# Performance work log

Hardware: AMD Instinct MI355X
Metric: run time of the kernel (lower is better)

The kernel has to match this reference:

```python
import jax, jax.numpy as jnp
import numpy as np

V, E, H, L = 50257, 256, 1024, 2   # vocab, embed_dim, hidden_dim, num_layers
B, T, K = 64, 80, 5                # batch, max_len, top_k
TEMP = 0.75
TWO_PI_OVER_24 = np.float32(2.0 * np.pi / 24.0)


def setup_inputs() -> dict:
    key = jax.random.key(0)
    ks = jax.random.split(key, 12)
    n = lambda i, shape, s: (jax.random.normal(ks[i], shape, jnp.float32) * s)
    hours = jax.random.uniform(ks[0], (B,), jnp.float32) * 24.0
    return {
        "hours": hours,
        "tp_w1": n(1, (2, H), 0.5),
        "tp_b1": jnp.zeros((H,), jnp.float32),
        "tp_w2": n(2, (H, 2 * L * H), 0.02),
        "tp_b2": jnp.zeros((2 * L * H,), jnp.float32),
        "embed": n(3, (V, E), 0.1).at[0].set(0.0),  # padding_idx=0 row zeroed
        "w_ih0": n(4, (E, 4 * H), 0.05),
        "w_hh0": n(5, (H, 4 * H), 0.05),
        "b0": jnp.zeros((4 * H,), jnp.float32),     # b_ih + b_hh combined
        "w_ih1": n(6, (H, 4 * H), 0.05),
        "w_hh1": n(7, (H, 4 * H), 0.05),
        "b1": jnp.zeros((4 * H,), jnp.float32),
        "fc_w": n(8, (H, V), 0.02),
        "fc_b": jnp.zeros((V,), jnp.float32),
        "sos_id": 1,
    }


def _lstm_cell(x, h, c, w_ih, w_hh, b):
    # torch gate order: i, f, g, o
    g = x @ w_ih + h @ w_hh + b
    i, f, gg, o = jnp.split(g, 4, axis=-1)
    c2 = jax.nn.sigmoid(f) * c + jax.nn.sigmoid(i) * jnp.tanh(gg)
    h2 = jax.nn.sigmoid(o) * jnp.tanh(c2)
    return h2, c2


def reference(hours, tp_w1, tp_b1, tp_w2, tp_b2, embed,
              w_ih0, w_hh0, b0, w_ih1, w_hh1, b1, fc_w, fc_b, sos_id):
    # _encode_time: sin/cos of hour angle -> MLP -> (h0, c0) per layer
    a = hours * TWO_PI_OVER_24
    feat = jnp.stack([jnp.sin(a), jnp.cos(a)], axis=-1)          # [B,2]
    tp = jnp.tanh(feat @ tp_w1 + tp_b1) @ tp_w2 + tp_b2          # [B,2*L*H]
    tp = tp.reshape(B, L, 2, H)
    h = jnp.transpose(tp[:, :, 0, :], (1, 0, 2))                 # [L,B,H]
    c = jnp.transpose(tp[:, :, 1, :], (1, 0, 2))                 # [L,B,H]

    keys = jax.random.split(jax.random.key(42), T)

    def step(carry, k):
        h, c, tok = carry
        x = embed[tok]                                           # [B,E]
        h0n, c0n = _lstm_cell(x, h[0], c[0], w_ih0, w_hh0, b0)
        h1n, c1n = _lstm_cell(h0n, h[1], c[1], w_ih1, w_hh1, b1)
        logits = (h1n @ fc_w + fc_b) / TEMP                      # [B,V]
        topv, topi = jax.lax.top_k(logits, K)                    # [B,K]
        probs = jax.nn.softmax(topv, axis=-1)
        sel = jax.random.categorical(k, topv, axis=-1)           # [B], == multinomial(probs)
        nxt = jnp.take_along_axis(topi, sel[:, None], axis=1)[:, 0]
        return (jnp.stack([h0n, h1n]), jnp.stack([c0n, c1n]), nxt), (nxt, probs)

    tok0 = jnp.full((B,), sos_id, jnp.int32)
    _, (toks, probs) = jax.lax.scan(step, (h, c, tok0), keys)
    # toks: [T,B] -> [B,T]; probs: [T,B,K] -> [B,T,K]
    return jnp.transpose(toks, (1, 0)), jnp.transpose(probs, (1, 0, 2))
```

## Files before the change

kernel.cpp:

```cpp
#include <hip/hip_runtime.h>
#include <math.h>
#include <stdint.h>
#include <limits.h>

#define VSZ 50257
#define ESZ 256
#define HSZ 1024
#define BSZ 64
#define TSZ 80
#define GC  4096
#define NFCB 786
#define NCAND (NFCB*5)
#define NSLOT 13
#define NREF 16

typedef unsigned int u32;
typedef unsigned short u16;
typedef double f64x4 __attribute__((ext_vector_type(4)));
typedef float f32x4v __attribute__((ext_vector_type(4)));
typedef __bf16 bf16x8 __attribute__((ext_vector_type(8)));
union BFrag { u16 u[8]; bf16x8 v; };

__device__ __forceinline__ u16 f2bf(float f) {
  u32 x = __float_as_uint(f);
  return (u16)((x + 0x7FFFu + ((x >> 16) & 1u)) >> 16);
}
__device__ __forceinline__ float bf2f(u16 h) { return __uint_as_float(((u32)h) << 16); }

__device__ __forceinline__ void tf2x32(u32 k0, u32 k1, u32& x0, u32& x1) {
  u32 ks2 = k0 ^ k1 ^ 0x1BD11BDAu;
  x0 += k0; x1 += k1;
#define RND(r) { x0 += x1; x1 = (x1 << r) | (x1 >> (32 - r)); x1 ^= x0; }
  RND(13) RND(15) RND(26) RND(6)
  x0 += k1; x1 += ks2 + 1u;
  RND(17) RND(29) RND(16) RND(24)
  x0 += ks2; x1 += k0 + 2u;
  RND(13) RND(15) RND(26) RND(6)
  x0 += k0; x1 += k1 + 3u;
  RND(17) RND(29) RND(16) RND(24)
  x0 += k1; x1 += ks2 + 4u;
  RND(13) RND(15) RND(26) RND(6)
  x0 += ks2; x1 += k0 + 5u;
#undef RND
}

__device__ __forceinline__ double dsig(double x) { return 0.5 + 0.5 * tanh(0.5 * x); }

__device__ __forceinline__ void ins5(double v, int i, double* tv, int* ti) {
  bool beat4 = (v > tv[4]) || (v == tv[4] && i < ti[4]);
  if (!beat4) return;
  tv[4] = v; ti[4] = i;
#pragma unroll
  for (int p = 4; p > 0; --p) {
    bool sw = (tv[p] > tv[p-1]) || (tv[p] == tv[p-1] && ti[p] < ti[p-1]);
    double a0 = sw ? tv[p] : tv[p-1]; double a1 = sw ? tv[p-1] : tv[p];
    tv[p-1] = a0; tv[p] = a1;
    int b0 = sw ? ti[p] : ti[p-1]; int b1 = sw ? ti[p-1] : ti[p];
    ti[p-1] = b0; ti[p] = b1;
  }
}

__device__ __forceinline__ double dref(int m, int n) {
  int s = 0;
#pragma unroll
  for (int k = 0; k < 4; ++k) s += (4*m + k + 1) * (16*k + n + 1);
  return (double)s;
}

__global__ __launch_bounds__(64) void k_probe(int* __restrict__ fbp) {
  int l = threadIdx.x;
  int lane16 = l & 15, sub = l >> 4;
  {
    double av = (double)(4 * lane16 + sub + 1);
    double bv = (double)(16 * sub + lane16 + 1);
    f64x4 acc = {0., 0., 0., 0.};
    acc = __builtin_amdgcn_mfma_f64_16x16x4f64(av, bv, acc, 0, 0, 0);
    bool o0 = true, o1 = true, o2 = true, o3 = true;
#pragma unroll
    for (int j = 0; j < 4; ++j) {
      double d = acc[j];
      o0 = o0 && (d == dref(4 * sub + j, lane16));
      o1 = o1 && (d == dref(lane16, 4 * sub + j));
      o2 = o2 && (d == dref(sub + 4 * j, lane16));
      o3 = o3 && (d == dref(lane16, sub + 4 * j));
    }
    int a0 = __all(o0), a1 = __all(o1), a2 = __all(o2), a3 = __all(o3);
    if (l == 0) { fbp[0] = a0 ? 0 : a1 ? 1 : a2 ? 2 : 3; fbp[1] = 0; }
  }
  {
    BFrag fa, fbv;
#pragma unroll
    for (int i = 0; i < 8; ++i) {
      int k = sub * 8 + i;
      fa.u[i]  = f2bf((float)((lane16 * 5 + k * 3) % 63 + 1));
      fbv.u[i] = f2bf((float)((k * 7 + lane16 * 11) % 61 + 1));
    }
    f32x4v c = {0.f, 0.f, 0.f, 0.f};
    c = __builtin_amdgcn_mfma_f32_16x16x32_bf16(fa.v, fbv.v, c, 0, 0, 0);
    bool okb = true;
#pragma unroll
    for (int j = 0; j < 4; ++j) {
      int mm = sub * 4 + j, nn = lane16;
      int ref = 0;
      for (int k = 0; k < 32; ++k) ref += ((mm*5 + k*3) % 63 + 1) * ((k*7 + nn*11) % 61 + 1);
      okb = okb && (c[j] == (float)ref);
    }
    int allb = __all(okb);
    if (l == 0) fbp[2] = allb;
  }
}

__global__ __launch_bounds__(256) void k_wconv(const float* __restrict__ W, u16* __restrict__ whT) {
  __shared__ u16 tile[64][65];
  int vb = blockIdx.x * 64, kb = blockIdx.y * 64;
  int tid = threadIdx.x;
#pragma unroll
  for (int i = 0; i < 16; ++i) {
    int r = i * 4 + (tid >> 6), c = tid & 63;
    int v = vb + c;
    tile[c][r] = (v < VSZ) ? f2bf(W[(size_t)(kb + r) * VSZ + v]) : (u16)0;
  }
  __syncthreads();
#pragma unroll
  for (int i = 0; i < 16; ++i) {
    int r = i * 4 + (tid >> 6), c = tid & 63;
    int v = vb + r;
    if (v < VSZ) whT[(size_t)v * 1024 + kb + c] = tile[r][c];
  }
}

__global__ __launch_bounds__(256) void k_rng(double* __restrict__ gum) {
  int idx = blockIdx.x * 256 + threadIdx.x;
  if (idx >= TSZ * 320) return;
  int t = idx / 320, m = idx % 320;
  u32 a0 = 0u, a1 = (u32)t;
  tf2x32(0u, 42u, a0, a1);
  u32 x0 = 0u, x1 = (u32)m;
  tf2x32(a0, a1, x0, x1);
  u32 bits = x0 ^ x1;
  const float TINY = 1.17549435082228750797e-38f;
  float f = __uint_as_float((bits >> 9) | 0x3f800000u) - 1.0f;
  float u = f + TINY;
  u = fmaxf(TINY, u);
  gum[idx] = -log(-log((double)u));
}

__global__ __launch_bounds__(256) void k_time1(const float* __restrict__ hours, const float* __restrict__ w1,
                                               const float* __restrict__ bb1, double* __restrict__ tp1T) {
  int idx = blockIdx.x * 256 + threadIdx.x;
  int b = idx & 63, hcol = idx >> 6;
  const float TPO = (float)(2.0 * 3.14159265358979323846 / 24.0);
  float af = hours[b] * TPO;
  double a = (double)af;
  double sv = sin(a), cv = cos(a);
  double vv = tanh(sv * (double)w1[hcol] + cv * (double)w1[HSZ + hcol] + (double)bb1[hcol]);
  tp1T[(size_t)hcol * 64 + b] = vv;
}

__global__ __launch_bounds__(256) void k_gemm_simple(const double* __restrict__ XTa, const float* __restrict__ Wa,
                                                     int Ka, int Sa, double* __restrict__ part) {
  int j = blockIdx.x * 256 + threadIdx.x;
  if (j >= GC) return;
  int s = blockIdx.y;
  int kc = Ka / Sa, k0 = s * kc;
  double acc[BSZ];
#pragma unroll
  for (int b = 0; b < BSZ; ++b) acc[b] = 0.0;
  const float* wp = Wa + (size_t)k0 * GC + j;
  const double* xp = XTa + (size_t)k0 * 64;
  for (int k = 0; k < kc; ++k) {
    double wv = (double)wp[0]; wp += GC;
#pragma unroll
    for (int b = 0; b < BSZ; ++b) acc[b] = fma(wv, xp[b], acc[b]);
    xp += 64;
  }
  double* o = part + ((size_t)s * 64) * GC + j;
#pragma unroll
  for (int b = 0; b < BSZ; ++b) o[(size_t)b * GC] = acc[b];
}

__global__ __launch_bounds__(256) void k_t2r(const double* __restrict__ part, const float* __restrict__ b2,
                                             double* __restrict__ h0T, double* __restrict__ c0,
                                             double* __restrict__ h1T, double* __restrict__ c1) {
  int b = blockIdx.y;
  int j = blockIdx.x * 256 + threadIdx.x;
  double acc = (double)b2[j];
  for (int s = 0; s < 8; ++s) acc += part[((size_t)s * 64 + b) * GC + j];
  int l = j >> 11, half = (j >> 10) & 1, hcol = j & 1023;
  if (half == 0) (l ? h1T : h0T)[(size_t)hcol * 64 + b] = acc;
  else           (l ? c1 : c0)[(size_t)b * HSZ + hcol] = acc;
}

__global__ __launch_bounds__(256, 4) void k_lstm_mfma(const double* __restrict__ x0, const float* __restrict__ W0,
                                                      const double* __restrict__ x1, const float* __restrict__ W1,
                                                      const double* __restrict__ x2, const float* __restrict__ W2,
                                                      int s1, int s2, double* __restrict__ part,
                                                      const int* __restrict__ fbp) {
  int conv = fbp[0] & 3;
  __shared__ double xs[64 * 64];
  int tid = threadIdx.x;
  int l = tid & 63, wv = tid >> 6;
  int sub = l >> 4, lane16 = l & 15;
  int colbase = blockIdx.x * 64;
  int s = blockIdx.y;
  const double* XT; const float* W; int k0;
  if (s < s1)      { XT = x0; W = W0; k0 = s * 256; }
  else if (s < s2) { XT = x1; W = W1; k0 = (s - s1) * 256; }
  else             { XT = x2; W = W2; k0 = (s - s2) * 256; }
  int colA = colbase + wv * 16 + lane16;
  f64x4 a0 = {0.,0.,0.,0.}, a1 = {0.,0.,0.,0.}, a2 = {0.,0.,0.,0.}, a3 = {0.,0.,0.,0.};
  const float* wp = W + (size_t)(k0 + sub) * GC + colA;
  float ab[8];
#pragma unroll
  for (int u = 0; u < 8; ++u) { ab[u] = wp[0]; wp += (size_t)4 * GC; }
  for (int ch = 0; ch < 4; ++ch) {
    __syncthreads();
    const double2* src = (const double2*)(XT + (size_t)(k0 + ch * 64) * 64);
    double2* dst = (double2*)xs;
    for (int i = tid; i < 2048; i += 256) dst[i] = src[i];
    __syncthreads();
#pragma unroll
    for (int g = 0; g < 2; ++g) {
#pragma unroll
      for (int u = 0; u < 8; ++u) {
        int ks = g * 8 + u;
        int step = ch * 16 + ks;
        float nv = 0.f;
        if (step + 8 < 64) nv = wp[0];
        wp += (size_t)4 * GC;
        double av = (double)ab[u];
        const double* bp = xs + (ks * 4 + sub) * 64 + lane16;
        double b0 = bp[0], b1 = bp[16], b2 = bp[32], b3 = bp[48];
        a0 = __builtin_amdgcn_mfma_f64_16x16x4f64(av, b0, a0, 0, 0, 0);
        a1 = __builtin_amdgcn_mfma_f64_16x16x4f64(av, b1, a1, 0, 0, 0);
        a2 = __builtin_amdgcn_mfma_f64_16x16x4f64(av, b2, a2, 0, 0, 0);
        a3 = __builtin_amdgcn_mfma_f64_16x16x4f64(av, b3, a3, 0, 0, 0);
        ab[u] = nv;
      }
    }
  }
#pragma unroll
  for (int j = 0; j < 4; ++j) {
    int m = (conv == 0) ? sub * 4 + j : (conv == 2) ? sub + 4 * j : lane16;
    int n = (conv == 0) ? lane16 : (conv == 2) ? lane16 : ((conv == 1) ? sub * 4 + j : sub + 4 * j);
    size_t base = ((size_t)s * 64 + n) * GC + colbase + wv * 16 + m;
    part[base]                   = a0[j];
    part[base + (size_t)16 * GC] = a1[j];
    part[base + (size_t)32 * GC] = a2[j];
    part[base + (size_t)48 * GC] = a3[j];
  }
}

__global__ __launch_bounds__(256) void k_cell(const double* __restrict__ part, int sBeg, int S,
                                              const float* __restrict__ bias,
                                              double* __restrict__ c, double* __restrict__ hT,
                                              int emit, u16* __restrict__ xh) {
  int b = blockIdx.y;
  int hcol = blockIdx.x * 256 + threadIdx.x;
  double gi = (double)bias[hcol];
  double gf = (double)bias[1024 + hcol];
  double gg = (double)bias[2048 + hcol];
  double go = (double)bias[3072 + hcol];
#pragma unroll 4
  for (int s = sBeg; s < sBeg + S; ++s) {
    const double* p = part + ((size_t)s * 64 + b) * GC;
    gi += p[hcol]; gf += p[1024 + hcol]; gg += p[2048 + hcol]; go += p[3072 + hcol];
  }
  size_t ci = (size_t)b * HSZ + hcol;
  double cn = dsig(gf) * c[ci] + dsig(gi) * tanh(gg);
  double hn = dsig(go) * tanh(cn);
  c[ci] = cn;
  hT[(size_t)hcol * 64 + b] = hn;
  if (emit)
    xh[(size_t)(hcol >> 7) * 8192 + (size_t)b * 128 + (hcol & 127)] = f2bf((float)hn);
}

__global__ __launch_bounds__(256, 4) void k_fcbf(const u16* __restrict__ xhg, const u16* __restrict__ whT,
                                                 const float* __restrict__ fcb,
                                                 double* __restrict__ candV, int* __restrict__ candI,
                                                 const int* __restrict__ fbp) {
  if (fbp[2] == 0) return;
  __shared__ double xs[64 * 64];
  u16* lx = (u16*)xs;
  int tid = threadIdx.x;
  int l = tid & 63, wv = tid >> 6;
  int sub = l >> 4, lane16 = l & 15;
  int vbase = blockIdx.x * 64;
  int colA = min(vbase + wv * 16 + lane16, VSZ - 1);
  const u16* wrow = whT + (size_t)colA * 1024;
  f32x4v acc0 = {0,0,0,0}, acc1 = {0,0,0,0}, acc2 = {0,0,0,0}, acc3 = {0,0,0,0};
  for (int ch = 0; ch < 8; ++ch) {
    bf16x8 wh0 = *(const bf16x8*)(wrow + ch * 128 + 0 * 32 + sub * 8);
    bf16x8 wh1 = *(const bf16x8*)(wrow + ch * 128 + 1 * 32 + sub * 8);
    bf16x8 wh2 = *(const bf16x8*)(wrow + ch * 128 + 2 * 32 + sub * 8);
    bf16x8 wh3 = *(const bf16x8*)(wrow + ch * 128 + 3 * 32 + sub * 8);
    __syncthreads();
    {
      const uint4* sg = (const uint4*)(xhg + (size_t)ch * 8192);
      uint4* dl = (uint4*)lx;
#pragma unroll
      for (int i = 0; i < 4; ++i) {
        int u = tid + i * 256;
        int bswz = u >> 4, g = u & 15;
        dl[(bswz << 4) | (g ^ (bswz & 7))] = sg[u];
      }
    }
    __syncthreads();
#pragma unroll
    for (int kt = 0; kt < 4; ++kt) {
      bf16x8 whv = (kt == 0) ? wh0 : (kt == 1) ? wh1 : (kt == 2) ? wh2 : wh3;
#define BT_STEP(BT, ACC) {                                                              \
        int bb = BT * 16 + lane16;                                                      \
        const bf16x8* bp2 = (const bf16x8*)lx + ((bb << 4) | ((kt * 4 + sub) ^ (bb & 7))); \
        ACC = __builtin_amdgcn_mfma_f32_16x16x32_bf16(whv, *bp2, ACC, 0, 0, 0); }
      BT_STEP(0, acc0)
      BT_STEP(1, acc1)
      BT_STEP(2, acc2)
      BT_STEP(3, acc3)
#undef BT_STEP
    }
  }
  __syncthreads();
#pragma unroll
  for (int j = 0; j < 4; ++j) {
    int vl = wv * 16 + sub * 4 + j;
    int v = vbase + vl;
    bool okv = (v < VSZ);
    double bi = okv ? (double)fcb[min(v, VSZ - 1)] : 0.0;
    int b0i = lane16, b1i = 16 + lane16, b2i = 32 + lane16, b3i = 48 + lane16;
    xs[b0i * 64 + ((vl + b0i) & 63)] = okv ? ((double)acc0[j] + bi) / 0.75 : -INFINITY;
    xs[b1i * 64 + ((vl + b1i) & 63)] = okv ? ((double)acc1[j] + bi) / 0.75 : -INFINITY;
    xs[b2i * 64 + ((vl + b2i) & 63)] = okv ? ((double)acc2[j] + bi) / 0.75 : -INFINITY;
    xs[b3i * 64 + ((vl + b3i) & 63)] = okv ? ((double)acc3[j] + bi) / 0.75 : -INFINITY;
  }
  __syncthreads();
  if (tid < 64) {
    int b = tid;
    double tv[5]; int ti[5];
#pragma unroll
    for (int p = 0; p < 5; ++p) { tv[p] = -INFINITY; ti[p] = INT_MAX; }
    for (int vl2 = 0; vl2 < 64; ++vl2)
      ins5(xs[b * 64 + ((vl2 + b) & 63)], vbase + vl2, tv, ti);
#pragma unroll
    for (int r = 0; r < 5; ++r) {
      candV[(size_t)b * NCAND + blockIdx.x * 5 + r] = tv[r];
      candI[(size_t)b * NCAND + blockIdx.x * 5 + r] = ti[r];
    }
  }
}

__global__ __launch_bounds__(256, 4) void k_fcf64(const double* __restrict__ h1T, const float* __restrict__ W,
                                                  const float* __restrict__ fcb,
                                                  double* __restrict__ candV, int* __restrict__ candI,
                                                  const int* __restrict__ fbp, int force) {
  if (!force && fbp[2] != 0) return;
  int conv = fbp[0] & 3;
  __shared__ double xs[64 * 64];
  int tid = threadIdx.x;
  int l = tid & 63, wv = tid >> 6;
  int sub = l >> 4, lane16 = l & 15;
  int vbase = blockIdx.x * 64;
  int colA = min(vbase + wv * 16 + lane16, VSZ - 1);
  f64x4 a0 = {0.,0.,0.,0.}, a1 = {0.,0.,0.,0.}, a2 = {0.,0.,0.,0.}, a3 = {0.,0.,0.,0.};
  const float* wp = W + (size_t)sub * VSZ + colA;
  float ab[8];
#pragma unroll
  for (int u = 0; u < 8; ++u) { ab[u] = wp[0]; wp += (size_t)4 * VSZ; }
  for (int ch = 0; ch < 16; ++ch) {
    __syncthreads();
    const double2* src = (const double2*)(h1T + (size_t)ch * 64 * 64);
    double2* dst = (double2*)xs;
    for (int i = tid; i < 2048; i += 256) dst[i] = src[i];
    __syncthreads();
#pragma unroll
    for (int g = 0; g < 2; ++g) {
#pragma unroll
      for (int u = 0; u < 8; ++u) {
        int ks = g * 8 + u;
        int step = ch * 16 + ks;
        float nv = 0.f;
        if (step + 8 < 256) nv = wp[0];
        wp += (size_t)4 * VSZ;
        double av = (double)ab[u];
        const double* bp = xs + (ks * 4 + sub) * 64 + lane16;
        double b0 = bp[0], b1 = bp[16], b2 = bp[32], b3 = bp[48];
        a0 = __builtin_amdgcn_mfma_f64_16x16x4f64(av, b0, a0, 0, 0, 0);
        a1 = __builtin_amdgcn_mfma_f64_16x16x4f64(av, b1, a1, 0, 0, 0);
        a2 = __builtin_amdgcn_mfma_f64_16x16x4f64(av, b2, a2, 0, 0, 0);
        a3 = __builtin_amdgcn_mfma_f64_16x16x4f64(av, b3, a3, 0, 0, 0);
        ab[u] = nv;
      }
    }
  }
  __syncthreads();
#pragma unroll
  for (int j = 0; j < 4; ++j) {
    int m = (conv == 0) ? sub * 4 + j : (conv == 2) ? sub + 4 * j : lane16;
    int n = (conv == 0) ? lane16 : (conv == 2) ? lane16 : ((conv == 1) ? sub * 4 + j : sub + 4 * j);
    int vl = wv * 16 + m;
    int v = vbase + vl;
    bool okv = (v < VSZ);
    double bi = okv ? (double)fcb[min(v, VSZ - 1)] : 0.0;
    int b0i = n, b1i = 16 + n, b2i = 32 + n, b3i = 48 + n;
    xs[b0i * 64 + ((vl + b0i) & 63)] = okv ? (a0[j] + bi) / 0.75 : -INFINITY;
    xs[b1i * 64 + ((vl + b1i) & 63)] = okv ? (a1[j] + bi) / 0.75 : -INFINITY;
    xs[b2i * 64 + ((vl + b2i) & 63)] = okv ? (a2[j] + bi) / 0.75 : -INFINITY;
    xs[b3i * 64 + ((vl + b3i) & 63)] = okv ? (a3[j] + bi) / 0.75 : -INFINITY;
  }
  __syncthreads();
  if (tid < 64) {
    int b = tid;
    double tv[5]; int ti[5];
#pragma unroll
    for (int p = 0; p < 5; ++p) { tv[p] = -INFINITY; ti[p] = INT_MAX; }
    for (int vl2 = 0; vl2 < 64; ++vl2)
      ins5(xs[b * 64 + ((vl2 + b) & 63)], vbase + vl2, tv, ti);
#pragma unroll
    for (int r = 0; r < 5; ++r) {
      candV[(size_t)b * NCAND + blockIdx.x * 5 + r] = tv[r];
      candI[(size_t)b * NCAND + blockIdx.x * 5 + r] = ti[r];
    }
  }
}

__global__ __launch_bounds__(256) void k_rfin(const double* __restrict__ candV, const int* __restrict__ candI,
                                              const float* __restrict__ W, const float* __restrict__ fcb,
                                              const double* __restrict__ h1T,
                                              const double* __restrict__ gum, int t,
                                              const float* __restrict__ embed,
                                              float* __restrict__ out, double* __restrict__ xt0) {
  __shared__ float sv[NCAND];
  __shared__ int   si[NCAND];
  __shared__ double exS[NREF];
  __shared__ float wvv[4]; __shared__ int wvi[4]; __shared__ int wvs[4];
  int b = blockIdx.x, tid = threadIdx.x;
  int l = tid & 63, wvd = tid >> 6;
  for (int e = tid; e < NCAND; e += 256) {
    sv[e] = (float)candV[(size_t)b * NCAND + e];
    si[e] = candI[(size_t)b * NCAND + e];
  }
  __syncthreads();
  int cidx[NREF];
#pragma unroll
  for (int r = 0; r < NREF; ++r) {
    float bv = -INFINITY; int bi = INT_MAX, bs = 0;
    for (int e = tid; e < NCAND; e += 256) {
      float v = sv[e]; int i2 = si[e];
      if (v > bv || (v == bv && i2 < bi)) { bv = v; bi = i2; bs = e; }
    }
#pragma unroll
    for (int off = 1; off < 64; off <<= 1) {
      float ov = __shfl_xor(bv, off, 64);
      int oi = __shfl_xor(bi, off, 64);
      int os = __shfl_xor(bs, off, 64);
      if (ov > bv || (ov == bv && oi < bi)) { bv = ov; bi = oi; bs = os; }
    }
    if (l == 0) { wvv[wvd] = bv; wvi[wvd] = bi; wvs[wvd] = bs; }
    __syncthreads();
    float fv = wvv[0]; int fi = wvi[0], fs = wvs[0];
#pragma unroll
    for (int q = 1; q < 4; ++q) {
      float ov = wvv[q]; int oi = wvi[q], os = wvs[q];
      if (ov > fv || (ov == fv && oi < fi)) { fv = ov; fi = oi; fs = os; }
    }
    cidx[r] = fi;
    __syncthreads();
    if (tid == 0) sv[fs] = -INFINITY;
    __syncthreads();
  }
#pragma unroll
  for (int rr = 0; rr < 4; ++rr) {
    int c = wvd + rr * 4;
    int vc = cidx[c];
    double p = 0.0;
#pragma unroll
    for (int i = 0; i < 16; ++i) {
      int k = i * 64 + l;
      p = fma((double)W[(size_t)k * VSZ + vc], h1T[(size_t)k * 64 + b], p);
    }
#pragma unroll
    for (int off = 1; off < 64; off <<= 1) p += __shfl_xor(p, off, 64);
    if (l == 0) exS[c] = (p + (double)fcb[vc]) / 0.75;
  }
  __syncthreads();
  double tv[5]; int ti[5];
#pragma unroll
  for (int p = 0; p < 5; ++p) { tv[p] = -INFINITY; ti[p] = INT_MAX; }
#pragma unroll
  for (int c = 0; c < NREF; ++c) ins5(exS[c], cidx[c], tv, ti);
  const double* g = gum + (size_t)t * 320 + b * 5;
  double bestv = tv[0] + g[0]; int best = 0;
#pragma unroll
  for (int k2 = 1; k2 < 5; ++k2) { double vv2 = tv[k2] + g[k2]; if (vv2 > bestv) { bestv = vv2; best = k2; } }
  int nxt = ti[best];
  if (tid == 0) {
    out[b * TSZ + t] = (float)nxt;
    double m = tv[0];
    double exx[5]; double s = 0.0;
#pragma unroll
    for (int k2 = 0; k2 < 5; ++k2) { exx[k2] = exp(tv[k2] - m); s += exx[k2]; }
    float* po = out + BSZ * TSZ + ((size_t)b * TSZ + t) * 5;
#pragma unroll
    for (int k2 = 0; k2 < 5; ++k2) po[k2] = (float)(exx[k2] / s);
  }
  xt0[(size_t)tid * 64 + b] = (double)embed[(size_t)nxt * ESZ + tid];
}

__global__ __launch_bounds__(256) void k_emb0(const float* __restrict__ embed, const int* __restrict__ sos,
                                              double* __restrict__ xt0) {
  int idx = blockIdx.x * 256 + threadIdx.x;
  int b = idx & 63, k = idx >> 6;
  xt0[(size_t)k * 64 + b] = (double)embed[(size_t)sos[0] * ESZ + k];
}

extern "C" void kernel_launch(void* const* d_in, const int* in_sizes, int n_in,
                              void* d_out, int out_size, void* d_ws, size_t ws_size,
                              hipStream_t stream) {
  const float* hours = (const float*)d_in[0];
  const float* tp_w1 = (const float*)d_in[1];
  const float* tp_b1 = (const float*)d_in[2];
  const float* tp_w2 = (const float*)d_in[3];
  const float* tp_b2 = (const float*)d_in[4];
  const float* embed = (const float*)d_in[5];
  const float* w_ih0 = (const float*)d_in[6];
  const float* w_hh0 = (const float*)d_in[7];
  const float* b0    = (const float*)d_in[8];
  const float* w_ih1 = (const float*)d_in[9];
  const float* w_hh1 = (const float*)d_in[10];
  const float* b1    = (const float*)d_in[11];
  const float* fc_w  = (const float*)d_in[12];
  const float* fc_b  = (const float*)d_in[13];
  const int*   sos   = (const int*)d_in[14];
  float* out = (float*)d_out;

  char* w = (char*)d_ws;
  double* part = (double*)w;  w += (size_t)NSLOT * 64 * GC * 8;
  double* xt0  = (double*)w;  w += (size_t)ESZ * 64 * 8;
  double* h0T  = (double*)w;  w += (size_t)HSZ * 64 * 8;
  double* h1T  = (double*)w;  w += (size_t)HSZ * 64 * 8;
  double* c0   = (double*)w;  w += (size_t)BSZ * HSZ * 8;
  double* c1   = (double*)w;  w += (size_t)BSZ * HSZ * 8;
  double* tp1T = (double*)w;  w += (size_t)HSZ * 64 * 8;
  double* gum  = (double*)w;  w += (size_t)TSZ * 320 * 8;
  double* candV = (double*)w; w += (size_t)BSZ * NCAND * 8;
  int*    candI = (int*)w;    w += (size_t)BSZ * NCAND * 4;
  int*    fbuf  = (int*)w;    w += 64;
  u16*    xhg   = (u16*)w;    w += (size_t)HSZ * 64 * 2;
  u16*    whT   = (u16*)w;    w += (size_t)VSZ * 1024 * 2;
  size_t need = (size_t)(w - (char*)d_ws);
  int useBF = (ws_size >= need) ? 1 : 0;

  k_probe<<<dim3(1), dim3(64), 0, stream>>>(fbuf);
  k_rng<<<dim3(100), dim3(256), 0, stream>>>(gum);
  k_time1<<<dim3(256), dim3(256), 0, stream>>>(hours, tp_w1, tp_b1, tp1T);
  k_gemm_simple<<<dim3(16, 8), dim3(256), 0, stream>>>(tp1T, tp_w2, 1024, 8, part);
  k_t2r<<<dim3(16, 64), dim3(256), 0, stream>>>(part, tp_b2, h0T, c0, h1T, c1);
  k_emb0<<<dim3(64), dim3(256), 0, stream>>>(embed, sos, xt0);
  if (useBF)
    k_wconv<<<dim3(786, 16), dim3(256), 0, stream>>>(fc_w, whT);

  double* part9 = part + (size_t)9 * 64 * GC;
  for (int t = 0; t < TSZ; ++t) {
    k_lstm_mfma<<<dim3(64, 9), dim3(256), 0, stream>>>(xt0, w_ih0, h0T, w_hh0, h1T, w_hh1, 1, 5, part, fbuf);
    k_cell<<<dim3(4, 64), dim3(256), 0, stream>>>(part, 0, 5, b0, c0, h0T, 0, xhg);
    k_lstm_mfma<<<dim3(64, 4), dim3(256), 0, stream>>>(h0T, w_ih1, h0T, w_ih1, h0T, w_ih1, 4, 4, part9, fbuf);
    k_cell<<<dim3(4, 64), dim3(256), 0, stream>>>(part, 5, 8, b1, c1, h1T, 1, xhg);
    if (useBF)
      k_fcbf<<<dim3(NFCB), dim3(256), 0, stream>>>(xhg, whT, fc_b, candV, candI, fbuf);
    k_fcf64<<<dim3(NFCB), dim3(256), 0, stream>>>(h1T, fc_w, fc_b, candV, candI, fbuf, useBF ? 0 : 1);
    k_rfin<<<dim3(64), dim3(256), 0, stream>>>(candV, candI, fc_w, fc_b, h1T, gum, t, embed, out, xt0);
  }
}
```

Before: 19.11 ms.

## Replace LSTM f64 MFMA with vector FMA, merge FC kernels, streamline reranking

The LSTM gate GEMM kernel drops f64 MFMA with its layout-probe-dependent output mapping. Each thread now computes a 4x4 register tile using scalar double FMAs, with the weight prefetch changed to match. The bf16 and f64 FC paths are merged into one kernel that picks a path at runtime, which saves a launch per step. The rerank kernel now selects candidates in registers with a two-level wave reduction instead of 16 block-wide passes over LDS with repeated barriers. The risk is lower FLOP throughput in the LSTM GEMM, since scalar FP64 FMA may be slower than the MFMA path it replaces.

After: 22.77 ms. 19.1% more time.

```diff
diff --git a/kernel.cpp b/kernel.cpp
--- a/kernel.cpp
+++ b/kernel.cpp
@@ -191,64 +191,65 @@
   else           (l ? c1 : c0)[(size_t)b * HSZ + hcol] = acc;
 }
 
-__global__ __launch_bounds__(256, 4) void k_lstm_mfma(const double* __restrict__ x0, const float* __restrict__ W0,
-                                                      const double* __restrict__ x1, const float* __restrict__ W1,
-                                                      const double* __restrict__ x2, const float* __restrict__ W2,
-                                                      int s1, int s2, double* __restrict__ part,
-                                                      const int* __restrict__ fbp) {
-  int conv = fbp[0] & 3;
+__global__ __launch_bounds__(256, 4) void k_lstm_vec(const double* __restrict__ x0, const float* __restrict__ W0,
+                                                     const double* __restrict__ x1, const float* __restrict__ W1,
+                                                     const double* __restrict__ x2, const float* __restrict__ W2,
+                                                     int s1, int s2, double* __restrict__ part) {
   __shared__ double xs[64 * 64];
   int tid = threadIdx.x;
-  int l = tid & 63, wv = tid >> 6;
-  int sub = l >> 4, lane16 = l & 15;
+  int vg = tid & 15, bg = tid >> 4;
   int colbase = blockIdx.x * 64;
   int s = blockIdx.y;
   const double* XT; const float* W; int k0;
   if (s < s1)      { XT = x0; W = W0; k0 = s * 256; }
   else if (s < s2) { XT = x1; W = W1; k0 = (s - s1) * 256; }
   else             { XT = x2; W = W2; k0 = (s - s2) * 256; }
-  int colA = colbase + wv * 16 + lane16;
-  f64x4 a0 = {0.,0.,0.,0.}, a1 = {0.,0.,0.,0.}, a2 = {0.,0.,0.,0.}, a3 = {0.,0.,0.,0.};
-  const float* wp = W + (size_t)(k0 + sub) * GC + colA;
-  float ab[8];
-#pragma unroll
-  for (int u = 0; u < 8; ++u) { ab[u] = wp[0]; wp += (size_t)4 * GC; }
+  double acc[4][4];
+#pragma unroll
+  for (int ci = 0; ci < 4; ++ci)
+#pragma unroll
+    for (int j = 0; j < 4; ++j) acc[ci][j] = 0.0;
+  const float* wp = W + (size_t)k0 * GC + colbase + vg;
+  float wb[4][4];
+#pragma unroll
+  for (int u = 0; u < 4; ++u) {
+    wb[u][0] = wp[0]; wb[u][1] = wp[16]; wb[u][2] = wp[32]; wb[u][3] = wp[48];
+    wp += GC;
+  }
   for (int ch = 0; ch < 4; ++ch) {
     __syncthreads();
     const double2* src = (const double2*)(XT + (size_t)(k0 + ch * 64) * 64);
     double2* dst = (double2*)xs;
     for (int i = tid; i < 2048; i += 256) dst[i] = src[i];
     __syncthreads();
-#pragma unroll
-    for (int g = 0; g < 2; ++g) {
-#pragma unroll
-      for (int u = 0; u < 8; ++u) {
-        int ks = g * 8 + u;
-        int step = ch * 16 + ks;
-        float nv = 0.f;
-        if (step + 8 < 64) nv = wp[0];
-        wp += (size_t)4 * GC;
-        double av = (double)ab[u];
-        const double* bp = xs + (ks * 4 + sub) * 64 + lane16;
-        double b0 = bp[0], b1 = bp[16], b2 = bp[32], b3 = bp[48];
-        a0 = __builtin_amdgcn_mfma_f64_16x16x4f64(av, b0, a0, 0, 0, 0);
-        a1 = __builtin_amdgcn_mfma_f64_16x16x4f64(av, b1, a1, 0, 0, 0);
-        a2 = __builtin_amdgcn_mfma_f64_16x16x4f64(av, b2, a2, 0, 0, 0);
-        a3 = __builtin_amdgcn_mfma_f64_16x16x4f64(av, b3, a3, 0, 0, 0);
-        ab[u] = nv;
+    for (int g = 0; g < 16; ++g) {
+#pragma unroll
+      for (int u = 0; u < 4; ++u) {
+        int step = ch * 64 + g * 4 + u;
+        float n0 = 0.f, n1 = 0.f, n2 = 0.f, n3 = 0.f;
+        if (step + 4 < 256) { n0 = wp[0]; n1 = wp[16]; n2 = wp[32]; n3 = wp[48]; }
+        wp += GC;
+        const double2* xp = (const double2*)(xs + (g * 4 + u) * 64 + (bg << 2));
+        double2 xa = xp[0], xb2 = xp[1];
+        double w0 = (double)wb[u][0], w1 = (double)wb[u][1];
+        double w2 = (double)wb[u][2], w3 = (double)wb[u][3];
+        acc[0][0] = fma(w0, xa.x, acc[0][0]);  acc[0][1] = fma(w0, xa.y, acc[0][1]);
+        acc[0][2] = fma(w0, xb2.x, acc[0][2]); acc[0][3] = fma(w0, xb2.y, acc[0][3]);
+        acc[1][0] = fma(w1, xa.x, acc[1][0]);  acc[1][1] = fma(w1, xa.y, acc[1][1]);
+        acc[1][2] = fma(w1, xb2.x, acc[1][2]); acc[1][3] = fma(w1, xb2.y, acc[1][3]);
+        acc[2][0] = fma(w2, xa.x, acc[2][0]);  acc[2][1] = fma(w2, xa.y, acc[2][1]);
+        acc[2][2] = fma(w2, xb2.x, acc[2][2]); acc[2][3] = fma(w2, xb2.y, acc[2][3]);
+        acc[3][0] = fma(w3, xa.x, acc[3][0]);  acc[3][1] = fma(w3, xa.y, acc[3][1]);
+        acc[3][2] = fma(w3, xb2.x, acc[3][2]); acc[3][3] = fma(w3, xb2.y, acc[3][3]);
+        wb[u][0] = n0; wb[u][1] = n1; wb[u][2] = n2; wb[u][3] = n3;
       }
     }
   }
 #pragma unroll
-  for (int j = 0; j < 4; ++j) {
-    int m = (conv == 0) ? sub * 4 + j : (conv == 2) ? sub + 4 * j : lane16;
-    int n = (conv == 0) ? lane16 : (conv == 2) ? lane16 : ((conv == 1) ? sub * 4 + j : sub + 4 * j);
-    size_t base = ((size_t)s * 64 + n) * GC + colbase + wv * 16 + m;
-    part[base]                   = a0[j];
-    part[base + (size_t)16 * GC] = a1[j];
-    part[base + (size_t)32 * GC] = a2[j];
-    part[base + (size_t)48 * GC] = a3[j];
-  }
+  for (int ci = 0; ci < 4; ++ci)
+#pragma unroll
+    for (int j = 0; j < 4; ++j)
+      part[((size_t)s * 64 + bg * 4 + j) * GC + colbase + vg + 16 * ci] = acc[ci][j];
 }
 
 __global__ __launch_bounds__(256) void k_cell(const double* __restrict__ part, int sBeg, int S,
@@ -275,137 +276,114 @@
     xh[(size_t)(hcol >> 7) * 8192 + (size_t)b * 128 + (hcol & 127)] = f2bf((float)hn);
 }
 
-__global__ __launch_bounds__(256, 4) void k_fcbf(const u16* __restrict__ xhg, const u16* __restrict__ whT,
-                                                 const float* __restrict__ fcb,
-                                                 double* __restrict__ candV, int* __restrict__ candI,
-                                                 const int* __restrict__ fbp) {
-  if (fbp[2] == 0) return;
-  __shared__ double xs[64 * 64];
-  u16* lx = (u16*)xs;
-  int tid = threadIdx.x;
-  int l = tid & 63, wv = tid >> 6;
-  int sub = l >> 4, lane16 = l & 15;
-  int vbase = blockIdx.x * 64;
-  int colA = min(vbase + wv * 16 + lane16, VSZ - 1);
-  const u16* wrow = whT + (size_t)colA * 1024;
-  f32x4v acc0 = {0,0,0,0}, acc1 = {0,0,0,0}, acc2 = {0,0,0,0}, acc3 = {0,0,0,0};
-  for (int ch = 0; ch < 8; ++ch) {
-    bf16x8 wh0 = *(const bf16x8*)(wrow + ch * 128 + 0 * 32 + sub * 8);
-    bf16x8 wh1 = *(const bf16x8*)(wrow + ch * 128 + 1 * 32 + sub * 8);
-    bf16x8 wh2 = *(const bf16x8*)(wrow + ch * 128 + 2 * 32 + sub * 8);
-    bf16x8 wh3 = *(const bf16x8*)(wrow + ch * 128 + 3 * 32 + sub * 8);
-    __syncthreads();
-    {
-      const uint4* sg = (const uint4*)(xhg + (size_t)ch * 8192);
-      uint4* dl = (uint4*)lx;
-#pragma unroll
-      for (int i = 0; i < 4; ++i) {
-        int u = tid + i * 256;
-        int bswz = u >> 4, g = u & 15;
-        dl[(bswz << 4) | (g ^ (bswz & 7))] = sg[u];
-      }
-    }
-    __syncthreads();
-#pragma unroll
-    for (int kt = 0; kt < 4; ++kt) {
-      bf16x8 whv = (kt == 0) ? wh0 : (kt == 1) ? wh1 : (kt == 2) ? wh2 : wh3;
-#define BT_STEP(BT, ACC) {                                                              \
-        int bb = BT * 16 + lane16;                                                      \
-        const bf16x8* bp2 = (const bf16x8*)lx + ((bb << 4) | ((kt * 4 + sub) ^ (bb & 7))); \
-        ACC = __builtin_amdgcn_mfma_f32_16x16x32_bf16(whv, *bp2, ACC, 0, 0, 0); }
-      BT_STEP(0, acc0)
-      BT_STEP(1, acc1)
-      BT_STEP(2, acc2)
-      BT_STEP(3, acc3)
-#undef BT_STEP
-    }
-  }
-  __syncthreads();
-#pragma unroll
-  for (int j = 0; j < 4; ++j) {
-    int vl = wv * 16 + sub * 4 + j;
-    int v = vbase + vl;
-    bool okv = (v < VSZ);
-    double bi = okv ? (double)fcb[min(v, VSZ - 1)] : 0.0;
-    int b0i = lane16, b1i = 16 + lane16, b2i = 32 + lane16, b3i = 48 + lane16;
-    xs[b0i * 64 + ((vl + b0i) & 63)] = okv ? ((double)acc0[j] + bi) / 0.75 : -INFINITY;
-    xs[b1i * 64 + ((vl + b1i) & 63)] = okv ? ((double)acc1[j] + bi) / 0.75 : -INFINITY;
-    xs[b2i * 64 + ((vl + b2i) & 63)] = okv ? ((double)acc2[j] + bi) / 0.75 : -INFINITY;
-    xs[b3i * 64 + ((vl + b3i) & 63)] = okv ? ((double)acc3[j] + bi) / 0.75 : -INFINITY;
-  }
-  __syncthreads();
-  if (tid < 64) {
-    int b = tid;
-    double tv[5]; int ti[5];
-#pragma unroll
-    for (int p = 0; p < 5; ++p) { tv[p] = -INFINITY; ti[p] = INT_MAX; }
-    for (int vl2 = 0; vl2 < 64; ++vl2)
-      ins5(xs[b * 64 + ((vl2 + b) & 63)], vbase + vl2, tv, ti);
-#pragma unroll
-    for (int r = 0; r < 5; ++r) {
-      candV[(size_t)b * NCAND + blockIdx.x * 5 + r] = tv[r];
-      candI[(size_t)b * NCAND + blockIdx.x * 5 + r] = ti[r];
-    }
-  }
-}
-
-__global__ __launch_bounds__(256, 4) void k_fcf64(const double* __restrict__ h1T, const float* __restrict__ W,
-                                                  const float* __restrict__ fcb,
-                                                  double* __restrict__ candV, int* __restrict__ candI,
-                                                  const int* __restrict__ fbp, int force) {
-  if (!force && fbp[2] != 0) return;
-  int conv = fbp[0] & 3;
+__global__ __launch_bounds__(256, 4) void k_fc(const u16* __restrict__ xhg, const u16* __restrict__ whT,
+                                               const double* __restrict__ h1T, const float* __restrict__ W,
+                                               const float* __restrict__ fcb,
+                                               double* __restrict__ candV, int* __restrict__ candI,
+                                               const int* __restrict__ fbp, int force) {
   __shared__ double xs[64 * 64];
   int tid = threadIdx.x;
   int l = tid & 63, wv = tid >> 6;
   int sub = l >> 4, lane16 = l & 15;
   int vbase = blockIdx.x * 64;
   int colA = min(vbase + wv * 16 + lane16, VSZ - 1);
-  f64x4 a0 = {0.,0.,0.,0.}, a1 = {0.,0.,0.,0.}, a2 = {0.,0.,0.,0.}, a3 = {0.,0.,0.,0.};
-  const float* wp = W + (size_t)sub * VSZ + colA;
-  float ab[8];
-#pragma unroll
-  for (int u = 0; u < 8; ++u) { ab[u] = wp[0]; wp += (size_t)4 * VSZ; }
-  for (int ch = 0; ch < 16; ++ch) {
+  bool bf = (!force) && (fbp[2] != 0);
+  if (bf) {
+    u16* lx = (u16*)xs;
+    const u16* wrow = whT + (size_t)colA * 1024;
+    f32x4v acc0 = {0,0,0,0}, acc1 = {0,0,0,0}, acc2 = {0,0,0,0}, acc3 = {0,0,0,0};
+    for (int ch = 0; ch < 8; ++ch) {
+      bf16x8 wh0 = *(const bf16x8*)(wrow + ch * 128 + 0 * 32 + sub * 8);
+      bf16x8 wh1 = *(const bf16x8*)(wrow + ch * 128 + 1 * 32 + sub * 8);
+      bf16x8 wh2 = *(const bf16x8*)(wrow + ch * 128 + 2 * 32 + sub * 8);
+      bf16x8 wh3 = *(const bf16x8*)(wrow + ch * 128 + 3 * 32 + sub * 8);
+      __syncthreads();
+      {
+        const uint4* sg = (const uint4*)(xhg + (size_t)ch * 8192);
+        uint4* dl = (uint4*)lx;
+#pragma unroll
+        for (int i = 0; i < 4; ++i) {
+          int u = tid + i * 256;
+          int bswz = u >> 4, g = u & 15;
+          dl[(bswz << 4) | (g ^ (bswz & 7))] = sg[u];
+        }
+      }
+      __syncthreads();
+#pragma unroll
+      for (int kt = 0; kt < 4; ++kt) {
+        bf16x8 whv = (kt == 0) ? wh0 : (kt == 1) ? wh1 : (kt == 2) ? wh2 : wh3;
+#define BT_STEP(BT, ACC) {                                                              \
+          int bb = BT * 16 + lane16;                                                    \
+          const bf16x8* bp2 = (const bf16x8*)lx + ((bb << 4) | ((kt * 4 + sub) ^ (bb & 7))); \
+          ACC = __builtin_amdgcn_mfma_f32_16x16x32_bf16(whv, *bp2, ACC, 0, 0, 0); }
+        BT_STEP(0, acc0)
+        BT_STEP(1, acc1)
+        BT_STEP(2, acc2)
+        BT_STEP(3, acc3)
+#undef BT_STEP
+      }
+    }
     __syncthreads();
-    const double2* src = (const double2*)(h1T + (size_t)ch * 64 * 64);
-    double2* dst = (double2*)xs;
-    for (int i = tid; i < 2048; i += 256) dst[i] = src[i];
+#pragma unroll
+    for (int j = 0; j < 4; ++j) {
+      int vl = wv * 16 + sub * 4 + j;
+      int v = vbase + vl;
+      bool okv = (v < VSZ);
+      double bi = okv ? (double)fcb[min(v, VSZ - 1)] : 0.0;
+      int b0i = lane16, b1i = 16 + lane16, b2i = 32 + lane16, b3i = 48 + lane16;
+      xs[b0i * 64 + ((vl + b0i) & 63)] = okv ? ((double)acc0[j] + bi) / 0.75 : -INFINITY;
+      xs[b1i * 64 + ((vl + b1i) & 63)] = okv ? ((double)acc1[j] + bi) / 0.75 : -INFINITY;
+      xs[b2i * 64 + ((vl + b2i) & 63)] = okv ? ((double)acc2[j] + bi) / 0.75 : -INFINITY;
+      xs[b3i * 64 + ((vl + b3i) & 63)] = okv ? ((double)acc3[j] + bi) / 0.75 : -INFINITY;
+    }
+  } else {
+    int conv = fbp[0] & 3;
+    f64x4 a0 = {0.,0.,0.,0.}, a1 = {0.,0.,0.,0.}, a2 = {0.,0.,0.,0.}, a3 = {0.,0.,0.,0.};
+    const float* wp = W + (size_t)sub * VSZ + colA;
+    float ab[8];
+#pragma unroll
+    for (int u = 0; u < 8; ++u) { ab[u] = wp[0]; wp += (size_t)4 * VSZ; }
+    for (int ch = 0; ch < 16; ++ch) {
+      __syncthreads();
+      const double2* src = (const double2*)(h1T + (size_t)ch * 64 * 64);
+      double2* dst = (double2*)xs;
+      for (int i = tid; i < 2048; i += 256) dst[i] = src[i];
+      __syncthreads();
+#pragma unroll
+      for (int g = 0; g < 2; ++g) {
+#pragma unroll
+        for (int u = 0; u < 8; ++u) {
+          int ks = g * 8 + u;
+          int step = ch * 16 + ks;
+          float nv = 0.f;
+          if (step + 8 < 256) nv = wp[0];
+          wp += (size_t)4 * VSZ;
+          double av = (double)ab[u];
+          const double* bp = xs + (ks * 4 + sub) * 64 + lane16;
+          double b0 = bp[0], b1 = bp[16], b2 = bp[32], b3 = bp[48];
+          a0 = __builtin_amdgcn_mfma_f64_16x16x4f64(av, b0, a0, 0, 0, 0);
+          a1 = __builtin_amdgcn_mfma_f64_16x16x4f64(av, b1, a1, 0, 0, 0);
+          a2 = __builtin_amdgcn_mfma_f64_16x16x4f64(av, b2, a2, 0, 0, 0);
+          a3 = __builtin_amdgcn_mfma_f64_16x16x4f64(av, b3, a3, 0, 0, 0);
+          ab[u] = nv;
+        }
+      }
+    }
     __syncthreads();
 #pragma unroll
-    for (int g = 0; g < 2; ++g) {
-#pragma unroll
-      for (int u = 0; u < 8; ++u) {
-        int ks = g * 8 + u;
-        int step = ch * 16 + ks;
-        float nv = 0.f;
-        if (step + 8 < 256) nv = wp[0];
-        wp += (size_t)4 * VSZ;
-        double av = (double)ab[u];
-        const double* bp = xs + (ks * 4 + sub) * 64 + lane16;
-        double b0 = bp[0], b1 = bp[16], b2 = bp[32], b3 = bp[48];
-        a0 = __builtin_amdgcn_mfma_f64_16x16x4f64(av, b0, a0, 0, 0, 0);
-        a1 = __builtin_amdgcn_mfma_f64_16x16x4f64(av, b1, a1, 0, 0, 0);
-        a2 = __builtin_amdgcn_mfma_f64_16x16x4f64(av, b2, a2, 0, 0, 0);
-        a3 = __builtin_amdgcn_mfma_f64_16x16x4f64(av, b3, a3, 0, 0, 0);
-        ab[u] = nv;
-      }
-    }
-  }
-  __syncthreads();
-#pragma unroll
-  for (int j = 0; j < 4; ++j) {
-    int m = (conv == 0) ? sub * 4 + j : (conv == 2) ? sub + 4 * j : lane16;
-    int n = (conv == 0) ? lane16 : (conv == 2) ? lane16 : ((conv == 1) ? sub * 4 + j : sub + 4 * j);
-    int vl = wv * 16 + m;
-    int v = vbase + vl;
-    bool okv = (v < VSZ);
-    double bi = okv ? (double)fcb[min(v, VSZ - 1)] : 0.0;
-    int b0i = n, b1i = 16 + n, b2i = 32 + n, b3i = 48 + n;
-    xs[b0i * 64 + ((vl + b0i) & 63)] = okv ? (a0[j] + bi) / 0.75 : -INFINITY;
-    xs[b1i * 64 + ((vl + b1i) & 63)] = okv ? (a1[j] + bi) / 0.75 : -INFINITY;
-    xs[b2i * 64 + ((vl + b2i) & 63)] = okv ? (a2[j] + bi) / 0.75 : -INFINITY;
-    xs[b3i * 64 + ((vl + b3i) & 63)] = okv ? (a3[j] + bi) / 0.75 : -INFINITY;
+    for (int j = 0; j < 4; ++j) {
+      int m = (conv == 0) ? sub * 4 + j : (conv == 2) ? sub + 4 * j : lane16;
+      int n = (conv == 0) ? lane16 : (conv == 2) ? lane16 : ((conv == 1) ? sub * 4 + j : sub + 4 * j);
+      int vl = wv * 16 + m;
+      int v = vbase + vl;
+      bool okv = (v < VSZ);
+      double bi = okv ? (double)fcb[min(v, VSZ - 1)] : 0.0;
+      int b0i = n, b1i = 16 + n, b2i = 32 + n, b3i = 48 + n;
+      xs[b0i * 64 + ((vl + b0i) & 63)] = okv ? (a0[j] + bi) / 0.75 : -INFINITY;
+      xs[b1i * 64 + ((vl + b1i) & 63)] = okv ? (a1[j] + bi) / 0.75 : -INFINITY;
+      xs[b2i * 64 + ((vl + b2i) & 63)] = okv ? (a2[j] + bi) / 0.75 : -INFINITY;
+      xs[b3i * 64 + ((vl + b3i) & 63)] = okv ? (a3[j] + bi) / 0.75 : -INFINITY;
+    }
   }
   __syncthreads();
   if (tid < 64) {
@@ -429,49 +407,57 @@
                                               const double* __restrict__ gum, int t,
                                               const float* __restrict__ embed,
                                               float* __restrict__ out, double* __restrict__ xt0) {
-  __shared__ float sv[NCAND];
-  __shared__ int   si[NCAND];
   __shared__ double exS[NREF];
-  __shared__ float wvv[4]; __shared__ int wvi[4]; __shared__ int wvs[4];
+  __shared__ float mv64[64]; __shared__ int mi64[64];
+  __shared__ int cidxS[NREF];
   int b = blockIdx.x, tid = threadIdx.x;
   int l = tid & 63, wvd = tid >> 6;
-  for (int e = tid; e < NCAND; e += 256) {
-    sv[e] = (float)candV[(size_t)b * NCAND + e];
-    si[e] = candI[(size_t)b * NCAND + e];
+  float v[16]; int ix[16];
+#pragma unroll
+  for (int q = 0; q < 16; ++q) {
+    int e = tid + q * 256;
+    if (e < NCAND) {
+      v[q] = (float)candV[(size_t)b * NCAND + e];
+      ix[q] = candI[(size_t)b * NCAND + e];
+    } else { v[q] = -INFINITY; ix[q] = INT_MAX; }
+  }
+#pragma unroll
+  for (int r = 0; r < 16; ++r) {
+    float bv = -INFINITY; int bi = INT_MAX; int bq = 0;
+#pragma unroll
+    for (int q = 0; q < 16; ++q)
+      if (v[q] > bv || (v[q] == bv && ix[q] < bi)) { bv = v[q]; bi = ix[q]; bq = q; }
+    float wv2 = bv; int wi = bi;
+#pragma unroll
+    for (int off = 1; off < 64; off <<= 1) {
+      float ov = __shfl_xor(wv2, off, 64);
+      int oi = __shfl_xor(wi, off, 64);
+      if (ov > wv2 || (ov == wv2 && oi < wi)) { wv2 = ov; wi = oi; }
+    }
+    if (bv == wv2 && bi == wi) { v[bq] = -INFINITY; ix[bq] = INT_MAX; }
+    if (l == 0) { mv64[wvd * 16 + r] = wv2; mi64[wvd * 16 + r] = wi; }
   }
   __syncthreads();
-  int cidx[NREF];
-#pragma unroll
-  for (int r = 0; r < NREF; ++r) {
-    float bv = -INFINITY; int bi = INT_MAX, bs = 0;
-    for (int e = tid; e < NCAND; e += 256) {
-      float v = sv[e]; int i2 = si[e];
-      if (v > bv || (v == bv && i2 < bi)) { bv = v; bi = i2; bs = e; }
-    }
-#pragma unroll
-    for (int off = 1; off < 64; off <<= 1) {
-      float ov = __shfl_xor(bv, off, 64);
-      int oi = __shfl_xor(bi, off, 64);
-      int os = __shfl_xor(bs, off, 64);
-      if (ov > bv || (ov == bv && oi < bi)) { bv = ov; bi = oi; bs = os; }
-    }
-    if (l == 0) { wvv[wvd] = bv; wvi[wvd] = bi; wvs[wvd] = bs; }
-    __syncthreads();
-    float fv = wvv[0]; int fi = wvi[0], fs = wvs[0];
-#pragma unroll
-    for (int q = 1; q < 4; ++q) {
-      float ov = wvv[q]; int oi = wvi[q], os = wvs[q];
-      if (ov > fv || (ov == fv && oi < fi)) { fv = ov; fi = oi; fs = os; }
-    }
-    cidx[r] = fi;
-    __syncthreads();
-    if (tid == 0) sv[fs] = -INFINITY;
-    __syncthreads();
-  }
+  if (wvd == 0) {
+    float cv = mv64[l]; int ci2 = mi64[l];
+#pragma unroll
+    for (int r = 0; r < NREF; ++r) {
+      float bv = cv; int bi = ci2;
+#pragma unroll
+      for (int off = 1; off < 64; off <<= 1) {
+        float ov = __shfl_xor(bv, off, 64);
+        int oi = __shfl_xor(bi, off, 64);
+        if (ov > bv || (ov == bv && oi < bi)) { bv = ov; bi = oi; }
+      }
+      if (cv == bv && ci2 == bi) { cv = -INFINITY; ci2 = INT_MAX; }
+      if (l == 0) cidxS[r] = bi;
+    }
+  }
+  __syncthreads();
 #pragma unroll
   for (int rr = 0; rr < 4; ++rr) {
     int c = wvd + rr * 4;
-    int vc = cidx[c];
+    int vc = cidxS[c];
     double p = 0.0;
 #pragma unroll
     for (int i = 0; i < 16; ++i) {
@@ -487,7 +473,7 @@
 #pragma unroll
   for (int p = 0; p < 5; ++p) { tv[p] = -INFINITY; ti[p] = INT_MAX; }
 #pragma unroll
-  for (int c = 0; c < NREF; ++c) ins5(exS[c], cidx[c], tv, ti);
+  for (int c = 0; c < NREF; ++c) ins5(exS[c], cidxS[c], tv, ti);
   const double* g = gum + (size_t)t * 320 + b * 5;
   double bestv = tv[0] + g[0]; int best = 0;
 #pragma unroll
@@ -561,13 +547,11 @@
 
   double* part9 = part + (size_t)9 * 64 * GC;
   for (int t = 0; t < TSZ; ++t) {
-    k_lstm_mfma<<<dim3(64, 9), dim3(256), 0, stream>>>(xt0, w_ih0, h0T, w_hh0, h1T, w_hh1, 1, 5, part, fbuf);
+    k_lstm_vec<<<dim3(64, 9), dim3(256), 0, stream>>>(xt0, w_ih0, h0T, w_hh0, h1T, w_hh1, 1, 5, part);
     k_cell<<<dim3(4, 64), dim3(256), 0, stream>>>(part, 0, 5, b0, c0, h0T, 0, xhg);
-    k_lstm_mfma<<<dim3(64, 4), dim3(256), 0, stream>>>(h0T, w_ih1, h0T, w_ih1, h0T, w_ih1, 4, 4, part9, fbuf);
+    k_lstm_vec<<<dim3(64, 4), dim3(256), 0, stream>>>(h0T, w_ih1, h0T, w_ih1, h0T, w_ih1, 4, 4, part9);
     k_cell<<<dim3(4, 64), dim3(256), 0, stream>>>(part, 5, 8, b1, c1, h1T, 1, xhg);
-    if (useBF)
-      k_fcbf<<<dim3(NFCB), dim3(256), 0, stream>>>(xhg, whT, fc_b, candV, candI, fbuf);
-    k_fcf64<<<dim3(NFCB), dim3(256), 0, stream>>>(h1T, fc_w, fc_b, candV, candI, fbuf, useBF ? 0 : 1);
+    k_fc<<<dim3(NFCB), dim3(256), 0, stream>>>(xhg, whT, h1T, fc_w, fc_b, candV, candI, fbuf, useBF ? 0 : 1);
     k_rfin<<<dim3(64), dim3(256), 0, stream>>>(candV, candI, fc_w, fc_b, h1T, gum, t, embed, out, xt0);
   }
 }
```
